# Kernel tuning notes

Measured on AMD Instinct MI355X. Metric: run time of the kernel, lower is better.

## Reference

```python
import jax, jax.numpy as jnp
import numpy as np


def build_mask_even(kh, kw):
    # Hexnet build_masks: zero one edge column for kernel rows at odd distance
    # from the kernel center (hex neighborhood); returns even-row mask + shift.
    mask = np.ones((kh, kw), dtype=np.float32)
    center = kh // 2
    shift = -1 if center % 2 else 1
    for r in range(kh):
        if abs(center - r) % 2:
            if shift == 1:
                mask[r, -1] = 0.0
            else:
                mask[r, 0] = 0.0
    return mask, shift


def setup_inputs() -> dict:
    key = jax.random.key(0)
    k1, k2, k3 = jax.random.split(key, 3)
    x = jax.random.normal(k1, (16, 128, 128, 128), dtype=jnp.float32)  # NHWC
    kernel = jax.random.normal(k2, (3, 3, 128, 256), dtype=jnp.float32) * 0.05  # HWIO
    bias = jax.random.normal(k3, (256,), dtype=jnp.float32) * 0.05
    return {"x": x, "kernel": kernel, "bias": bias}


def _hconv(x, kernel, bias):
    kh, kw = kernel.shape[0], kernel.shape[1]
    mask_np, shift = build_mask_even(kh, kw)
    kernel_even = kernel * jnp.asarray(mask_np)[:, :, None, None]

    # Odd-row kernel: only the rows at odd distance from center, rolled along width.
    center = kh // 2
    odd_rows = [jnp.roll(kernel_even[r], shift, axis=0)
                for r in range(kh) if abs(center - r) % 2]
    kernel_odd = jnp.stack(odd_rows, axis=0)  # (n_odd, kw, Cin, F)

    dn = ("NHWC", "HWIO", "NHWC")
    strides = (2, 1)  # build() doubles the H stride
    out_even = jax.lax.conv_general_dilated(
        x, kernel_even, window_strides=strides, padding="SAME",
        dimension_numbers=dn)
    out_odd = jax.lax.conv_general_dilated(
        x[:, 1:], kernel_odd, window_strides=strides, padding="SAME",
        dimension_numbers=dn)

    # Interleave rows: even0, odd0, even1, odd1, ... (+ trailing even row if longer)
    he, ho = out_even.shape[1], out_odd.shape[1]
    hm = min(he, ho)
    b, _, w, f = out_even.shape
    out = jnp.stack([out_even[:, :hm], out_odd[:, :hm]], axis=2)
    out = out.reshape(b, 2 * hm, w, f)
    if he > ho:
        out = jnp.concatenate([out, out_even[:, -1:]], axis=1)

    return jax.nn.relu(out + bias)


def reference(x, kernel, bias):
    return _hconv(x, kernel, bias)
```

## Files before the change

kernel.cpp:

```cpp
#include <hip/hip_runtime.h>


#define N_  16
#define H_  128
#define W_  128
#define C_  128
#define F_  256
#define HP  130
#define WP  130

typedef short bf16x8 __attribute__((ext_vector_type(8)));
typedef float f32x4  __attribute__((ext_vector_type(4)));

__device__ __forceinline__ unsigned int bf_bits(float f) {
  unsigned int u = __float_as_uint(f);
  return (u + 0x7FFFu + ((u >> 16) & 1u)) >> 16;
}
__device__ __forceinline__ unsigned int pack2(float a, float b) {
  return bf_bits(a) | (bf_bits(b) << 16);
}

__device__ __forceinline__ void even_tap(int ti, int& dr, int& dc, int& kr, int& kc) {
  switch (ti) {
    case 0:  dr = 0; dc = 0;  kr = 0; kc = 1; break;
    case 1:  dr = 0; dc = 1;  kr = 0; kc = 2; break;
    case 2:  dr = 1; dc = -1; kr = 1; kc = 0; break;
    case 3:  dr = 1; dc = 0;  kr = 1; kc = 1; break;
    case 4:  dr = 1; dc = 1;  kr = 1; kc = 2; break;
    case 5:  dr = 2; dc = 0;  kr = 2; kc = 1; break;
    default: dr = 2; dc = 1;  kr = 2; kc = 2; break;
  }
}

__global__ __launch_bounds__(256) void prep_xpad(
    const float* __restrict__ x, char* __restrict__ xpad) {
  long id = (long)blockIdx.x * 256 + threadIdx.x;
  const long total = (long)N_ * HP * WP * 16;
  if (id >= total) return;
  const int g  = (int)(id & 7);
  const int hc = (int)((id >> 3) & 1);
  long pix = id >> 4;
  const int wp = (int)(pix % WP);
  long t = pix / WP;
  const int hh = (int)(t % HP);
  const int nn = (int)(t / HP);
  const int ww = wp - 1;
  const int key = ww & 7;
  uint4 o = make_uint4(0u, 0u, 0u, 0u);
  if (hh < H_ && ww >= 0 && ww < W_) {
    const float* s = x + (((long)(nn * H_ + hh) * W_ + ww) * C_ + hc * 64 + (g ^ key) * 8);
    float4 a = *(const float4*)s;
    float4 b = *(const float4*)(s + 4);
    o.x = pack2(a.x, a.y); o.y = pack2(a.z, a.w);
    o.z = pack2(b.x, b.y); o.w = pack2(b.z, b.w);
  }
  *(uint4*)(xpad + id * 16) = o;
}

__global__ __launch_bounds__(256) void prep_wt2(
    const float* __restrict__ k, char* __restrict__ wt2) {
  int id = blockIdx.x * 256 + threadIdx.x;
  if (id >= 7 * 2 * 2 * 128 * 8) return;
  const int g  = id & 7;
  const int f  = (id >> 3) & 127;
  const int ft = (id >> 10) & 1;
  const int hc = (id >> 11) & 1;
  const int ti = id >> 12;
  int dr, dc, kr, kc;
  even_tap(ti, dr, dc, kr, kc);
  const int fg = ft * 128 + f;
  const int c0 = hc * 64 + (g ^ (f & 7)) * 8;
  float v[8];
#pragma unroll
  for (int j = 0; j < 8; ++j)
    v[j] = k[((size_t)(kr * 3 + kc) * C_ + (c0 + j)) * F_ + fg];
  uint4 o;
  o.x = pack2(v[0], v[1]); o.y = pack2(v[2], v[3]);
  o.z = pack2(v[4], v[5]); o.w = pack2(v[6], v[7]);
  *(uint4*)(wt2 + (size_t)id * 16) = o;
}

__global__ __launch_bounds__(256, 2) void hconv_mfma(
    const char* __restrict__ xpad,
    const char* __restrict__ wt2,
    const float* __restrict__ bias,
    float* __restrict__ out) {
  __shared__ __align__(16) char smem[65536];

  const int tid = threadIdx.x;
  const int bid = (blockIdx.x & 7) * 512 + (blockIdx.x >> 3);
  const int ft = bid & 1;
  const int h  = (bid >> 1) & 127;
  const int n  = bid >> 8;
  const int p  = h & 1;
  const int nsteps = p ? 8 : 14;

  const int lane = tid & 63;
  const int wid  = tid >> 6;
  const int wr   = wid >> 1;
  const int wc   = wid & 1;
  const int l16  = lane & 15;
  const int lk   = lane >> 4;

  auto step_info = [&](int s, int& dc, int& widx, int& dr) {
    if (p == 0) {
      int ti = s >> 1; widx = ti;
      int kr, kc; even_tap(ti, dr, dc, kr, kc);
    } else {
      int q = s >> 1;
      dr = q >> 1;
      dc = (q & 1) ? 0 : -1;
      widx = (q == 0) ? 0 : (q == 1) ? 1 : (q == 2) ? 5 : 6;
    }
  };

  auto stage = [&](int s, int sel) {
    int dc, widx, dr; step_info(s, dc, widx, dr);
    const int hc = s & 1;
    const long rowbase = (long)(n * HP + (h + dr)) * WP;
#pragma unroll
    for (int i = 0; i < 4; ++i) {
      const int L = i * 256 + tid;
      const int row = L >> 3, slot = L & 7;
      const char* src = xpad + (rowbase + (row + dc + 1)) * 256 + hc * 128 + slot * 16;
      __builtin_amdgcn_global_load_lds(
          (const __attribute__((address_space(1))) void*)src,
          (__attribute__((address_space(3))) void*)(smem + sel * 16384 + L * 16),
          16, 0, 0);
    }
    const char* bsrc = wt2 + (size_t)((widx * 2 + hc) * 2 + ft) * 16384;
#pragma unroll
    for (int i = 0; i < 4; ++i) {
      const int L = i * 256 + tid;
      __builtin_amdgcn_global_load_lds(
          (const __attribute__((address_space(1))) void*)(bsrc + L * 16),
          (__attribute__((address_space(3))) void*)(smem + 32768 + sel * 16384 + L * 16),
          16, 0, 0);
    }
  };

  f32x4 acc[4][4] = {};

  stage(0, 0);
  __syncthreads();

  for (int s = 0; s < nsteps; ++s) {
    const int cur = s & 1;
    if (s + 1 < nsteps) stage(s + 1, cur ^ 1);

    int dc, widx, dr; step_info(s, dc, widx, dr);
    const char* ab = (const char*)smem + cur * 16384;
    const char* bb = (const char*)smem + 32768 + cur * 16384;

    bf16x8 af[4][2], bfr[4][2];
#pragma unroll
    for (int m = 0; m < 4; ++m) {
      const int wl  = wr * 64 + m * 16 + l16;
      const int key = (wl + dc) & 7;
#pragma unroll
      for (int kk = 0; kk < 2; ++kk)
        af[m][kk] = *(const bf16x8*)(ab + wl * 128 + (((kk * 4 + lk) ^ key) * 16));
    }
#pragma unroll
    for (int fi = 0; fi < 4; ++fi) {
      const int fl = wc * 64 + fi * 16 + l16;
#pragma unroll
      for (int kk = 0; kk < 2; ++kk)
        bfr[fi][kk] = *(const bf16x8*)(bb + fl * 128 + (((kk * 4 + lk) ^ (fl & 7)) * 16));
    }

#pragma unroll
    for (int m = 0; m < 4; ++m)
#pragma unroll
      for (int fi = 0; fi < 4; ++fi)
#pragma unroll
        for (int kk = 0; kk < 2; ++kk)
          acc[m][fi] = __builtin_amdgcn_mfma_f32_16x16x32_bf16(
              af[m][kk], bfr[fi][kk], acc[m][fi], 0, 0, 0);

    __syncthreads();
  }

#pragma unroll
  for (int fi = 0; fi < 4; ++fi) {
    const int f = ft * 128 + wc * 64 + fi * 16 + l16;
    const float bv = bias[f];
#pragma unroll
    for (int m = 0; m < 4; ++m) {
      const int w = wr * 64 + m * 16 + lk * 4;
      float* o = out + (((size_t)(n * H_ + h) * W_ + w) * F_ + f);
#pragma unroll
      for (int r = 0; r < 4; ++r) {
        float v = acc[m][fi][r] + bv;
        v = v > 0.f ? v : 0.f;
        o[(size_t)r * F_] = v;
      }
    }
  }
}

__device__ __forceinline__ void tap_info11(int t, int& dr, int& dc, int& kr, int& kc) {
  switch (t) {
    case 0:  dr = 0; dc = 0;  kr = 0; kc = 1; break;
    case 1:  dr = 0; dc = 1;  kr = 0; kc = 2; break;
    case 2:  dr = 1; dc = -1; kr = 1; kc = 0; break;
    case 3:  dr = 1; dc = 0;  kr = 1; kc = 1; break;
    case 4:  dr = 1; dc = 1;  kr = 1; kc = 2; break;
    case 5:  dr = 2; dc = 0;  kr = 2; kc = 1; break;
    case 6:  dr = 2; dc = 1;  kr = 2; kc = 2; break;
    case 7:  dr = 0; dc = -1; kr = 0; kc = 1; break;
    case 8:  dr = 0; dc = 0;  kr = 0; kc = 2; break;
    case 9:  dr = 1; dc = -1; kr = 2; kc = 1; break;
    default: dr = 1; dc = 0;  kr = 2; kc = 2; break;
  }
}

__global__ __launch_bounds__(256) void build_w_fb(
    const float* __restrict__ k, unsigned short* __restrict__ wt) {
  int tid = blockIdx.x * 256 + threadIdx.x;
  if (tid >= 11 * F_ * C_) return;
  int c = tid & 127;
  int f = (tid >> 7) & 255;
  int t = tid >> 15;
  int dr, dc, kr, kc;
  tap_info11(t, dr, dc, kr, kc);
  wt[tid] = (unsigned short)bf_bits(k[((kr * 3 + kc) * C_ + c) * F_ + f]);
}

__global__ __launch_bounds__(256, 3) void hconv_fb(
    const float* __restrict__ x,
    const unsigned short* __restrict__ wt,
    const float* __restrict__ bias,
    float* __restrict__ out) {
  __shared__ __align__(16) char smem[49152];
  const int tid = threadIdx.x;
  const int bid = (blockIdx.x & 7) * 1024 + (blockIdx.x >> 3);
  const int ft    = bid & 1;
  const int wtile = (bid >> 1) & 1;
  const int h     = (bid >> 2) & 127;
  const int n     = bid >> 9;
  const int f0 = ft * 128;
  const int w0 = wtile * 64;
  const int p  = h & 1;
  const int tap0   = p ? 7 : 0;
  const int nsteps = p ? 8 : 14;
  const int lane = tid & 63;
  const int wid  = tid >> 6;
  const int l16  = lane & 15;
  const int lk   = lane >> 4;
  const int awl = tid >> 2;
  const int ag2 = tid & 3;
  const int bfl   = tid >> 1;
  const int bhalf = tid & 1;
  float4 ar0, ar1, ar2, ar3;
  uint4  br0, br1, br2, br3;
  auto load_step = [&](int s) {
    const int tap = tap0 + (s >> 1);
    const int cc  = s & 1;
    int dr, dc, kr, kc;
    tap_info11(tap, dr, dc, kr, kc);
    const int hh = h + dr;
    const int wg = w0 + awl + dc;
    const bool av = (hh < H_) && (wg >= 0) && (wg < W_);
    if (av) {
      const float* ap = x + (((long)(n * H_ + hh) * W_ + wg) * C_ + cc * 64 + ag2 * 16);
      ar0 = *(const float4*)(ap);
      ar1 = *(const float4*)(ap + 4);
      ar2 = *(const float4*)(ap + 8);
      ar3 = *(const float4*)(ap + 12);
    } else {
      ar0 = ar1 = ar2 = ar3 = make_float4(0.f, 0.f, 0.f, 0.f);
    }
    const unsigned short* bp =
        wt + ((size_t)(tap * F_ + f0 + bfl) * C_ + cc * 64 + bhalf * 32);
    const uint4* bq = (const uint4*)bp;
    br0 = bq[0]; br1 = bq[1]; br2 = bq[2]; br3 = bq[3];
  };
  auto write_step = [&](int sel) {
    uint4 u0, u1;
    u0.x = pack2(ar0.x, ar0.y); u0.y = pack2(ar0.z, ar0.w);
    u0.z = pack2(ar1.x, ar1.y); u0.w = pack2(ar1.z, ar1.w);
    u1.x = pack2(ar2.x, ar2.y); u1.y = pack2(ar2.z, ar2.w);
    u1.z = pack2(ar3.x, ar3.y); u1.w = pack2(ar3.z, ar3.w);
    char* abase = (char*)smem + sel * 8192 + awl * 128;
    const int sw = awl & 7;
    *(uint4*)(abase + (((2 * ag2)     ^ sw) * 16)) = u0;
    *(uint4*)(abase + (((2 * ag2 + 1) ^ sw) * 16)) = u1;
    char* bbase = (char*)smem + 16384 + sel * 16384 + bfl * 128;
    const int sb = bfl & 7;
    *(uint4*)(bbase + (((bhalf * 4 + 0) ^ sb) * 16)) = br0;
    *(uint4*)(bbase + (((bhalf * 4 + 1) ^ sb) * 16)) = br1;
    *(uint4*)(bbase + (((bhalf * 4 + 2) ^ sb) * 16)) = br2;
    *(uint4*)(bbase + (((bhalf * 4 + 3) ^ sb) * 16)) = br3;
  };
  f32x4 acc[4][2] = {};
  load_step(0);
  write_step(0);
  load_step(1);
  __syncthreads();
  for (int s = 0; s < nsteps; ++s) {
    const int cur = s & 1;
    const char* ab = (const char*)smem + cur * 8192;
    const char* bb = (const char*)smem + 16384 + cur * 16384;
    bf16x8 af[4][2], bfr[2][2];
#pragma unroll
    for (int m = 0; m < 4; ++m)
#pragma unroll
      for (int kkk = 0; kkk < 2; ++kkk) {
        const int wl = m * 16 + l16;
        const int g  = (kkk * 4 + lk) ^ (wl & 7);
        af[m][kkk] = *(const bf16x8*)(ab + wl * 128 + g * 16);
      }
#pragma unroll
    for (int fi = 0; fi < 2; ++fi)
#pragma unroll
      for (int kkk = 0; kkk < 2; ++kkk) {
        const int fl = wid * 32 + fi * 16 + l16;
        const int g  = (kkk * 4 + lk) ^ (fl & 7);
        bfr[fi][kkk] = *(const bf16x8*)(bb + fl * 128 + g * 16);
      }
    if (s + 1 < nsteps) write_step(cur ^ 1);
    if (s + 2 < nsteps) load_step(s + 2);
#pragma unroll
    for (int m = 0; m < 4; ++m)
#pragma unroll
      for (int fi = 0; fi < 2; ++fi)
#pragma unroll
        for (int kkk = 0; kkk < 2; ++kkk)
          acc[m][fi] = __builtin_amdgcn_mfma_f32_16x16x32_bf16(
              af[m][kkk], bfr[fi][kkk], acc[m][fi], 0, 0, 0);
    __syncthreads();
  }
#pragma unroll
  for (int fi = 0; fi < 2; ++fi) {
    const int f = f0 + wid * 32 + fi * 16 + l16;
    const float bv = bias[f];
#pragma unroll
    for (int m = 0; m < 4; ++m) {
      const int w = w0 + m * 16 + lk * 4;
      float* o = out + (((size_t)(n * H_ + h) * W_ + w) * F_ + f);
#pragma unroll
      for (int r = 0; r < 4; ++r) {
        float v = acc[m][fi][r] + bv;
        v = v > 0.f ? v : 0.f;
        o[(size_t)r * F_] = v;
      }
    }
  }
}

extern "C" void kernel_launch(void* const* d_in, const int* in_sizes, int n_in,
                              void* d_out, int out_size, void* d_ws, size_t ws_size,
                              hipStream_t stream) {
  const float* x    = (const float*)d_in[0];
  const float* kern = (const float*)d_in[1];
  const float* bias = (const float*)d_in[2];
  float* out = (float*)d_out;

  const size_t XPAD_BYTES = (size_t)N_ * HP * WP * 256;
  const size_t WT2_BYTES  = (size_t)7 * 2 * 2 * 128 * 8 * 16;

  if (ws_size >= XPAD_BYTES + WT2_BYTES) {
    char* xpad = (char*)d_ws;
    char* wt2  = (char*)d_ws + XPAD_BYTES;
    {
      const long total = (long)N_ * HP * WP * 16;
      prep_xpad<<<(int)((total + 255) / 256), 256, 0, stream>>>(x, xpad);
    }
    prep_wt2<<<112, 256, 0, stream>>>(kern, wt2);
    hconv_mfma<<<N_ * H_ * 2, 256, 0, stream>>>(xpad, wt2, bias, out);
  } else {
    unsigned short* wt = (unsigned short*)d_ws;
    build_w_fb<<<(11 * F_ * C_ + 255) / 256, 256, 0, stream>>>(kern, wt);
    hconv_fb<<<N_ * H_ * 2 * 2, 256, 0, stream>>>(x, wt, bias, out);
  }
}
```

Before: 170.2 us.

## Triple-buffer K=32 chunks with merged A/B tiles and async-waitcnt pipeline

```diff
diff --git a/kernel.cpp b/kernel.cpp
--- a/kernel.cpp
+++ b/kernel.cpp
@@ -37,18 +37,16 @@
   long id = (long)blockIdx.x * 256 + threadIdx.x;
   const long total = (long)N_ * HP * WP * 16;
   if (id >= total) return;
-  const int g  = (int)(id & 7);
-  const int hc = (int)((id >> 3) & 1);
+  const int g  = (int)(id & 15);
   long pix = id >> 4;
   const int wp = (int)(pix % WP);
   long t = pix / WP;
   const int hh = (int)(t % HP);
   const int nn = (int)(t / HP);
   const int ww = wp - 1;
-  const int key = ww & 7;
   uint4 o = make_uint4(0u, 0u, 0u, 0u);
   if (hh < H_ && ww >= 0 && ww < W_) {
-    const float* s = x + (((long)(nn * H_ + hh) * W_ + ww) * C_ + hc * 64 + (g ^ key) * 8);
+    const float* s = x + (((long)(nn * H_ + hh) * W_ + ww) * C_ + g * 8);
     float4 a = *(const float4*)s;
     float4 b = *(const float4*)(s + 4);
     o.x = pack2(a.x, a.y); o.y = pack2(a.z, a.w);
@@ -57,35 +55,33 @@
   *(uint4*)(xpad + id * 16) = o;
 }
 
-__global__ __launch_bounds__(256) void prep_wt2(
-    const float* __restrict__ k, char* __restrict__ wt2) {
+__global__ __launch_bounds__(256) void prep_wt3(
+    const float* __restrict__ k, char* __restrict__ wt3) {
   int id = blockIdx.x * 256 + threadIdx.x;
-  if (id >= 7 * 2 * 2 * 128 * 8) return;
-  const int g  = id & 7;
-  const int f  = (id >> 3) & 127;
-  const int ft = (id >> 10) & 1;
-  const int hc = (id >> 11) & 1;
+  if (id >= 7 * 4 * 256 * 4) return;
+  const int j  = id & 3;
+  const int f  = (id >> 2) & 255;
+  const int cq = (id >> 10) & 3;
   const int ti = id >> 12;
   int dr, dc, kr, kc;
   even_tap(ti, dr, dc, kr, kc);
-  const int fg = ft * 128 + f;
-  const int c0 = hc * 64 + (g ^ (f & 7)) * 8;
+  const int c0 = cq * 32 + j * 8;
   float v[8];
 #pragma unroll
-  for (int j = 0; j < 8; ++j)
-    v[j] = k[((size_t)(kr * 3 + kc) * C_ + (c0 + j)) * F_ + fg];
+  for (int m = 0; m < 8; ++m)
+    v[m] = k[((size_t)(kr * 3 + kc) * C_ + (c0 + m)) * F_ + f];
   uint4 o;
   o.x = pack2(v[0], v[1]); o.y = pack2(v[2], v[3]);
   o.z = pack2(v[4], v[5]); o.w = pack2(v[6], v[7]);
-  *(uint4*)(wt2 + (size_t)id * 16) = o;
-}
-
-__global__ __launch_bounds__(256, 2) void hconv_mfma(
+  *(uint4*)(wt3 + (size_t)id * 16) = o;
+}
+
+__global__ __launch_bounds__(256, 3) void hconv_mfma(
     const char* __restrict__ xpad,
-    const char* __restrict__ wt2,
+    const char* __restrict__ wt3,
     const float* __restrict__ bias,
     float* __restrict__ out) {
-  __shared__ __align__(16) char smem[65536];
+  __shared__ __align__(16) char smem[49152];
 
   const int tid = threadIdx.x;
   const int bid = (blockIdx.x & 7) * 512 + (blockIdx.x >> 3);
@@ -93,7 +89,7 @@
   const int h  = (bid >> 1) & 127;
   const int n  = bid >> 8;
   const int p  = h & 1;
-  const int nsteps = p ? 8 : 14;
+  const int nsteps = p ? 16 : 28;
 
   const int lane = tid & 63;
   const int wid  = tid >> 6;
@@ -104,10 +100,10 @@
 
   auto step_info = [&](int s, int& dc, int& widx, int& dr) {
     if (p == 0) {
-      int ti = s >> 1; widx = ti;
+      int ti = s >> 2; widx = ti;
       int kr, kc; even_tap(ti, dr, dc, kr, kc);
     } else {
-      int q = s >> 1;
+      int q = s >> 2;
       dr = q >> 1;
       dc = (q & 1) ? 0 : -1;
       widx = (q == 0) ? 0 : (q == 1) ? 1 : (q == 2) ? 5 : 6;
@@ -116,69 +112,60 @@
 
   auto stage = [&](int s, int sel) {
     int dc, widx, dr; step_info(s, dc, widx, dr);
-    const int hc = s & 1;
-    const long rowbase = (long)(n * HP + (h + dr)) * WP;
+    const int cq = s & 3;
+    const char* arow = xpad + ((long)(n * HP + (h + dr)) * WP + (dc + 1)) * 256 + cq * 64;
+    const char* brow = wt3 + ((size_t)((widx * 4 + cq) * 256 + ft * 128)) * 64;
+    char* dst0 = (char*)smem + sel * 16384;
 #pragma unroll
     for (int i = 0; i < 4; ++i) {
       const int L = i * 256 + tid;
-      const int row = L >> 3, slot = L & 7;
-      const char* src = xpad + (rowbase + (row + dc + 1)) * 256 + hc * 128 + slot * 16;
+      const int r = L >> 3, g = L & 7;
+      const int l = g ^ (r & 7);
+      const char* srcA = arow + (long)r * 256 + l * 16;
+      const char* srcB = brow + r * 64 + (l - 4) * 16;
+      const char* src = (l < 4) ? srcA : srcB;
       __builtin_amdgcn_global_load_lds(
           (const __attribute__((address_space(1))) void*)src,
-          (__attribute__((address_space(3))) void*)(smem + sel * 16384 + L * 16),
-          16, 0, 0);
-    }
-    const char* bsrc = wt2 + (size_t)((widx * 2 + hc) * 2 + ft) * 16384;
-#pragma unroll
-    for (int i = 0; i < 4; ++i) {
-      const int L = i * 256 + tid;
-      __builtin_amdgcn_global_load_lds(
-          (const __attribute__((address_space(1))) void*)(bsrc + L * 16),
-          (__attribute__((address_space(3))) void*)(smem + 32768 + sel * 16384 + L * 16),
-          16, 0, 0);
+          (__attribute__((address_space(3))) void*)(dst0 + L * 16), 16, 0, 0);
     }
   };
 
   f32x4 acc[4][4] = {};
 
   stage(0, 0);
-  __syncthreads();
+  if (nsteps > 1) stage(1, 1);
 
   for (int s = 0; s < nsteps; ++s) {
-    const int cur = s & 1;
-    if (s + 1 < nsteps) stage(s + 1, cur ^ 1);
-
-    int dc, widx, dr; step_info(s, dc, widx, dr);
-    const char* ab = (const char*)smem + cur * 16384;
-    const char* bb = (const char*)smem + 32768 + cur * 16384;
-
-    bf16x8 af[4][2], bfr[4][2];
+    const int sel = s % 3;
+    if (s + 1 < nsteps) {
+      asm volatile("s_waitcnt vmcnt(4)" ::: "memory");
+    } else {
+      asm volatile("s_waitcnt vmcnt(0)" ::: "memory");
+    }
+    __builtin_amdgcn_s_barrier();
+    if (s + 2 < nsteps) stage(s + 2, (s + 2) % 3);
+
+    const char* tb = (const char*)smem + sel * 16384;
+    bf16x8 af[4], bfr[4];
 #pragma unroll
     for (int m = 0; m < 4; ++m) {
-      const int wl  = wr * 64 + m * 16 + l16;
-      const int key = (wl + dc) & 7;
-#pragma unroll
-      for (int kk = 0; kk < 2; ++kk)
-        af[m][kk] = *(const bf16x8*)(ab + wl * 128 + (((kk * 4 + lk) ^ key) * 16));
+      const int wl = wr * 64 + m * 16 + l16;
+      af[m] = *(const bf16x8*)(tb + wl * 128 + ((lk ^ (wl & 7)) * 16));
     }
 #pragma unroll
     for (int fi = 0; fi < 4; ++fi) {
       const int fl = wc * 64 + fi * 16 + l16;
-#pragma unroll
-      for (int kk = 0; kk < 2; ++kk)
-        bfr[fi][kk] = *(const bf16x8*)(bb + fl * 128 + (((kk * 4 + lk) ^ (fl & 7)) * 16));
-    }
-
+      bfr[fi] = *(const bf16x8*)(tb + fl * 128 + (((4 + lk) ^ (fl & 7)) * 16));
+    }
+
+    __builtin_amdgcn_s_setprio(1);
 #pragma unroll
     for (int m = 0; m < 4; ++m)
 #pragma unroll
       for (int fi = 0; fi < 4; ++fi)
-#pragma unroll
-        for (int kk = 0; kk < 2; ++kk)
-          acc[m][fi] = __builtin_amdgcn_mfma_f32_16x16x32_bf16(
-              af[m][kk], bfr[fi][kk], acc[m][fi], 0, 0, 0);
-
-    __syncthreads();
+        acc[m][fi] = __builtin_amdgcn_mfma_f32_16x16x32_bf16(
+            af[m], bfr[fi], acc[m][fi], 0, 0, 0);
+    __builtin_amdgcn_s_setprio(0);
   }
 
 #pragma unroll
@@ -358,17 +345,17 @@
   float* out = (float*)d_out;
 
   const size_t XPAD_BYTES = (size_t)N_ * HP * WP * 256;
-  const size_t WT2_BYTES  = (size_t)7 * 2 * 2 * 128 * 8 * 16;
-
-  if (ws_size >= XPAD_BYTES + WT2_BYTES) {
+  const size_t WT3_BYTES  = (size_t)7 * 4 * 256 * 4 * 16;
+
+  if (ws_size >= XPAD_BYTES + WT3_BYTES) {
     char* xpad = (char*)d_ws;
-    char* wt2  = (char*)d_ws + XPAD_BYTES;
+    char* wt3  = (char*)d_ws + XPAD_BYTES;
     {
       const long total = (long)N_ * HP * WP * 16;
       prep_xpad<<<(int)((total + 255) / 256), 256, 0, stream>>>(x, xpad);
     }
-    prep_wt2<<<112, 256, 0, stream>>>(kern, wt2);
-    hconv_mfma<<<N_ * H_ * 2, 256, 0, stream>>>(xpad, wt2, bias, out);
+    prep_wt3<<<(7 * 4 * 256 * 4 + 255) / 256, 256, 0, stream>>>(kern, wt3);
+    hconv_mfma<<<N_ * H_ * 2, 256, 0, stream>>>(xpad, wt3, bias, out);
   } else {
     unsigned short* wt = (unsigned short*)d_ws;
     build_w_fb<<<(11 * F_ * C_ + 255) / 256, 256, 0, stream>>>(kern, wt);
```

Result: slower. 175.9 us (+3.3%).
